# Performance work log

Measured on AMD Instinct MI355X. Metric: run time of the kernel, lower is better.

Reference implementation:

```python
import jax, jax.numpy as jnp
import numpy as np

N_NODES = 79
RAW_FEAT = 26
D_IN = RAW_FEAT + 6      # 32, in_channels after position concat
D_OUT = 2 * D_IN         # 64, out_channel_fac * in_channels
HIDDEN = 256
N_EDGES = 3000
BATCH = 256
POS_IDX = [120,124,128,132,136,140,144,148,152,237,241,245,249,253,257,261,265,269,354,358,362,366,370,374,378,382,386,471,475,479,483,487,491,495,499,503,588,592,596,600,604,608,612,616,620,705,709,713,717,721,725,729,733,737,822,826,830,834,838,842,846,850,854,48,53,60,67,73,157,352,388,583,586,817,901,906,913,920,926]


def _positions():
    width, height = 39, 25
    p = np.asarray(POS_IDX)
    xn = (p % width) / (width - 1)
    yn = (p // width) / (height - 1)
    feats = np.stack([xn, yn,
                      (np.sin(xn * 2 * np.pi) + 1) / 2,
                      (np.cos(xn * 2 * np.pi) + 1) / 2,
                      (np.sin(yn * 2 * np.pi) + 1) / 2,
                      (np.cos(yn * 2 * np.pi) + 1) / 2], axis=-1)
    return jnp.asarray(feats, jnp.float32)


def setup_inputs() -> dict:
    key = jax.random.key(0)
    ks = jax.random.split(key, 20)
    s = 0.05
    inp = {
        "state": jax.random.normal(ks[0], (BATCH, N_NODES, RAW_FEAT), jnp.float32),
        "pos_feat": _positions(),
        "edge_weights": jax.random.uniform(ks[1], (N_EDGES, 1), jnp.float32),
        # TransformerConv params (heads=1, edge_dim=1): torch Linear weights [out,in]
        "Wq": jax.random.normal(ks[2], (D_OUT, D_IN)) * s, "bq": jnp.zeros((D_OUT,)),
        "Wk": jax.random.normal(ks[3], (D_OUT, D_IN)) * s, "bk": jnp.zeros((D_OUT,)),
        "Wv": jax.random.normal(ks[4], (D_OUT, D_IN)) * s, "bv": jnp.zeros((D_OUT,)),
        "We": jax.random.normal(ks[5], (D_OUT, 1)) * s,            # lin_edge, bias=False
        "Wskip": jax.random.normal(ks[6], (D_OUT, D_IN)) * s, "bskip": jnp.zeros((D_OUT,)),
        # MLP head
        "W1": jax.random.normal(ks[7], (HIDDEN, D_IN + D_OUT + 1)) * s, "b1": jnp.zeros((HIDDEN,)),
        "g1": jnp.ones((HIDDEN,)), "beta1": jnp.zeros((HIDDEN,)),
        "W2": jax.random.normal(ks[8], (HIDDEN, HIDDEN)) * s, "b2": jnp.zeros((HIDDEN,)),
        "g2": jnp.ones((HIDDEN,)), "beta2": jnp.zeros((HIDDEN,)),
        "W3": jax.random.normal(ks[9], (1, HIDDEN)) * s, "b3": jnp.zeros((1,)),
        "edge_index": jax.random.randint(ks[10], (2, N_EDGES), 0, N_NODES, jnp.int32),
    }
    return inp


def _layernorm(x, g, b):
    m = x.mean(-1, keepdims=True)
    v = ((x - m) ** 2).mean(-1, keepdims=True)
    return (x - m) / jnp.sqrt(v + 1e-5) * g + b


def reference(state, pos_feat, edge_weights, Wq, bq, Wk, bk, Wv, bv, We, Wskip, bskip,
              W1, b1, g1, beta1, W2, b2, g2, beta2, W3, b3, edge_index):
    B = state.shape[0]
    # concat normalized positional features (shared across batch)
    x = jnp.concatenate([state, jnp.broadcast_to(pos_feat, (B, N_NODES, 6))], -1)  # [B,N,D_IN]
    src, dst = edge_index[0], edge_index[1]
    e = edge_weights @ We.T  # [E, D_OUT] edge embedding, shared across batch
    scale = 1.0 / jnp.sqrt(jnp.float32(D_OUT))

    def conv_one(xg):  # TransformerConv, heads=1, concat, root_weight
        q = xg @ Wq.T + bq
        k = xg @ Wk.T + bk
        v = xg @ Wv.T + bv
        ke = k[src] + e                      # [E, D_OUT]
        ve = v[src] + e
        alpha = (q[dst] * ke).sum(-1) * scale  # [E]
        amax = jax.ops.segment_max(alpha, dst, num_segments=N_NODES)
        amax = jnp.where(jnp.isfinite(amax), amax, 0.0)
        ex = jnp.exp(alpha - amax[dst])
        den = jax.ops.segment_sum(ex, dst, num_segments=N_NODES)
        w = ex / (den[dst] + 1e-16)
        agg = jax.ops.segment_sum(ve * w[:, None], dst, num_segments=N_NODES)
        return agg + xg @ Wskip.T + bskip

    out1 = jax.nn.relu(jax.vmap(conv_one)(x))  # [B,N,D_OUT]
    total_agents = x[..., 1].sum(-1)[:, None, None]  # [B,1,1]
    h = jnp.concatenate([out1, jnp.broadcast_to(total_agents, (B, N_NODES, 1)), x], -1)
    h = jax.nn.leaky_relu(_layernorm(h @ W1.T + b1, g1, beta1))
    h = jax.nn.leaky_relu(_layernorm(h @ W2.T + b2, g2, beta2))
    conc = jax.nn.softplus(h @ W3.T + b3).squeeze(-1)  # [B,N]
    action = conc / (conc.sum(-1, keepdims=True) + 1e-20)  # deterministic path
    return action
```

## Files before the change

### kernel.cpp

```cpp
#include <hip/hip_runtime.h>
#include <hip/hip_bf16.h>

#define N_NODES 79
#define RAW_FEAT 26
#define D_IN 32
#define D_OUT 64
#define HIDDEN 256
#define N_EDGES 3000
#define BATCH 256
#define M_ROWS (BATCH * N_NODES)
#define K1PAD 112

__global__ __launch_bounds__(256) void k_prep(
    const float* __restrict__ W1, const float* __restrict__ W2,
    const int* __restrict__ ei, const float* __restrict__ ew,
    const float* __restrict__ Wq, const float* __restrict__ Wk,
    const float* __restrict__ Wv, const float* __restrict__ Wsk,
    const float* __restrict__ bq, const float* __restrict__ bk,
    const float* __restrict__ bv, const float* __restrict__ bsk,
    float* __restrict__ W1t, float* __restrict__ W2t,
    float* __restrict__ Wall_t, float* __restrict__ ball,
    int* __restrict__ rp, int* __restrict__ csr_src,
    int* __restrict__ csr_dst, float* __restrict__ csr_ew)
{
    __shared__ float tile[64][65];
    __shared__ int cnt[N_NODES];
    __shared__ int base[N_NODES + 1];
    const int tid = threadIdx.x, bid = blockIdx.x;

    if (bid < 24) {
        const float* in; float* out; int C, Kpad, kb, rb;
        if (bid < 8) { in = W1; out = W1t; C = 97; Kpad = K1PAD;
                       kb = (bid & 1) * 64; rb = (bid >> 1) * 64; }
        else         { int b = bid - 8; in = W2; out = W2t; C = 256; Kpad = 256;
                       kb = (b & 3) * 64; rb = (b >> 2) * 64; }
        for (int i = tid; i < 4096; i += 256) {
            int rr = i >> 6, kk = i & 63;
            int r = rb + rr, k = kb + kk;
            tile[rr][kk] = (k < C) ? in[r * C + k] : 0.f;
        }
        __syncthreads();
        for (int i = tid; i < 4096; i += 256) {
            int kk = i >> 6, rr = i & 63;
            int k = kb + kk, r = rb + rr;
            if (k < Kpad) out[(size_t)k * HIDDEN + r] = tile[rr][kk];
        }
        return;
    }

    if (bid == 25) {
        for (int t = tid; t < 32 * 256; t += 256) {
            int k = t >> 8, j = t & 255;
            float v;
            if (j < 64)       v = Wq [j * 32 + k];
            else if (j < 128) v = Wk [(j - 64) * 32 + k];
            else if (j < 192) v = Wv [(j - 128) * 32 + k];
            else              v = Wsk[(j - 192) * 32 + k];
            Wall_t[t] = v;
        }
        if (tid < 64) {
            ball[tid]       = bq[tid];
            ball[64 + tid]  = bk[tid];
            ball[128 + tid] = bv[tid];
            ball[192 + tid] = bsk[tid];
        }
        return;
    }

    if (tid < N_NODES) cnt[tid] = 0;
    __syncthreads();
    for (int e = tid; e < N_EDGES; e += 256) atomicAdd(&cnt[ei[N_EDGES + e]], 1);
    __syncthreads();
    if (tid == 0) {
        int run = 0;
        for (int n = 0; n < N_NODES; ++n) { base[n] = run; run += cnt[n]; }
        base[N_NODES] = run;
    }
    __syncthreads();
    if (tid < N_NODES + 1) rp[tid] = base[tid];
    if (tid < N_NODES) cnt[tid] = base[tid];
    __syncthreads();
    for (int e = tid; e < N_EDGES; e += 256) {
        int d = ei[N_EDGES + e];
        int p = atomicAdd(&cnt[d], 1);
        csr_src[p] = ei[e];
        csr_dst[p] = d;
        csr_ew[p]  = ew[e];
    }
}

#define DOT4(S, Aa, Bb) S += Aa.x * Bb.x + Aa.y * Bb.y + Aa.z * Bb.z + Aa.w * Bb.w;

__global__ __launch_bounds__(512) void k1_conv(
    const float* __restrict__ state, const float* __restrict__ pos,
    const float* __restrict__ Wall_t, const float* __restrict__ ball,
    const int* __restrict__ rp_g, const int* __restrict__ csrc_g,
    const int* __restrict__ cdst_g, const float* __restrict__ cew_g,
    const float* __restrict__ We,
    float* __restrict__ out1_ws, float* __restrict__ ta_ws)
{
    __shared__ __align__(16) float qs [80 * 68];
    __shared__ __align__(16) float kss[80 * 68];
    __shared__ __align__(16) float vss[80 * 68];
    __shared__ __align__(16) float o1s[N_NODES * 68];
    __shared__ __align__(16) char uni[43904];
    __shared__ __align__(16) float ewc[N_EDGES];
    __shared__ unsigned short srcs[N_EDGES], dsts[N_EDGES];
    __shared__ __align__(16) float eW[64];
    __shared__ int   rp_s[80];
    __shared__ float qWe[80], csum_s[80];
    __shared__ float red80[80];

    float* xs     = (float*)uni;
    float* Wall_s = (float*)(uni + 10112);
    float* ball_s = (float*)(uni + 42880);
    float* SA     = (float*)uni;
    float* alpha  = (float*)(uni + 25600);

    const int b = blockIdx.x, tid = threadIdx.x;

    for (int t = tid; t < N_NODES * 32; t += 512) {
        int n = t >> 5, c = t & 31;
        xs[t] = (c < RAW_FEAT) ? state[(b * N_NODES + n) * RAW_FEAT + c]
                               : pos[n * 6 + (c - RAW_FEAT)];
    }
    {
        const float4* Wg4 = (const float4*)Wall_t;
        float4* Ws4w = (float4*)Wall_s;
        for (int t = tid; t < 2048; t += 512) Ws4w[t] = Wg4[t];
    }
    if (tid < 256) ball_s[tid] = ball[tid];
    for (int t = tid; t < N_EDGES; t += 512) {
        srcs[t] = (unsigned short)csrc_g[t];
        dsts[t] = (unsigned short)cdst_g[t];
        ewc[t]  = cew_g[t];
    }
    if (tid < 64) eW[tid] = We[tid];
    if (tid < 80) rp_s[tid] = rp_g[tid];
    if (tid < 79) red80[tid] = state[(b * N_NODES + tid) * RAW_FEAT + 1];
    if (tid == 79) red80[79] = 0.f;
    for (int t = tid; t < 68; t += 512) {
        qs[79 * 68 + t] = 0.f; kss[79 * 68 + t] = 0.f; vss[79 * 68 + t] = 0.f;
    }
    __syncthreads();

    {
        const float4* xs4 = (const float4*)xs;
        const float4* W4  = (const float4*)Wall_s;
        const float4* b4  = (const float4*)ball_s;
        for (int t = tid; t < N_NODES * 64; t += 512) {
            int n = t >> 6, c4 = t & 63;
            float4 acc = b4[c4];
            #pragma unroll
            for (int k4 = 0; k4 < 8; ++k4) {
                float4 xv = xs4[n * 8 + k4];
                float4 w0 = W4[(k4 * 4 + 0) * 64 + c4];
                float4 w1 = W4[(k4 * 4 + 1) * 64 + c4];
                float4 w2 = W4[(k4 * 4 + 2) * 64 + c4];
                float4 w3 = W4[(k4 * 4 + 3) * 64 + c4];
                acc.x += xv.x * w0.x + xv.y * w1.x + xv.z * w2.x + xv.w * w3.x;
                acc.y += xv.x * w0.y + xv.y * w1.y + xv.z * w2.y + xv.w * w3.y;
                acc.z += xv.x * w0.z + xv.y * w1.z + xv.z * w2.z + xv.w * w3.z;
                acc.w += xv.x * w0.w + xv.y * w1.w + xv.z * w2.w + xv.w * w3.w;
            }
            if (c4 < 16)      ((float4*)qs )[n * 17 + c4]        = acc;
            else if (c4 < 32) ((float4*)kss)[n * 17 + (c4 - 16)] = acc;
            else if (c4 < 48) ((float4*)vss)[n * 17 + (c4 - 32)] = acc;
            else              ((float4*)o1s)[n * 17 + (c4 - 48)] = acc;
        }
    }
    __syncthreads();

    for (int off = 64; off >= 1; off >>= 1) {
        if (tid < off && tid + off < 80) red80[tid] += red80[tid + off];
        __syncthreads();
    }
    if (tid == 0) ta_ws[b] = red80[0];
    if (tid < N_NODES) {
        const float4* q4 = (const float4*)(qs + tid * 68);
        const float4* e4 = (const float4*)eW;
        float s = 0.f;
        #pragma unroll
        for (int i = 0; i < 16; ++i) {
            float4 a = q4[i], e = e4[i];
            DOT4(s, a, e)
        }
        qWe[tid] = s;
    }
    __syncthreads();

    {
        const int rg = tid >> 5, cgp = tid & 31;
        const int r0 = rg * 5;
        int c0 = cgp * 3; if (c0 > 76) c0 = 76;
        float s00 = 0, s01 = 0, s02 = 0;
        float s10 = 0, s11 = 0, s12 = 0;
        float s20 = 0, s21 = 0, s22 = 0;
        float s30 = 0, s31 = 0, s32 = 0;
        float s40 = 0, s41 = 0, s42 = 0;
        const float4* q4p = (const float4*)qs;
        const float4* k4p = (const float4*)kss;
        for (int k4 = 0; k4 < 16; ++k4) {
            float4 q0 = q4p[(r0 + 0) * 17 + k4];
            float4 q1 = q4p[(r0 + 1) * 17 + k4];
            float4 q2 = q4p[(r0 + 2) * 17 + k4];
            float4 q3 = q4p[(r0 + 3) * 17 + k4];
            float4 q4v = q4p[(r0 + 4) * 17 + k4];
            float4 c0v = k4p[(c0 + 0) * 17 + k4];
            float4 c1v = k4p[(c0 + 1) * 17 + k4];
            float4 c2v = k4p[(c0 + 2) * 17 + k4];
            DOT4(s00, q0, c0v)  DOT4(s01, q0, c1v)  DOT4(s02, q0, c2v)
            DOT4(s10, q1, c0v)  DOT4(s11, q1, c1v)  DOT4(s12, q1, c2v)
            DOT4(s20, q2, c0v)  DOT4(s21, q2, c1v)  DOT4(s22, q2, c2v)
            DOT4(s30, q3, c0v)  DOT4(s31, q3, c1v)  DOT4(s32, q3, c2v)
            DOT4(s40, q4v, c0v) DOT4(s41, q4v, c1v) DOT4(s42, q4v, c2v)
        }
        SA[(r0 + 0) * 80 + c0 + 0] = s00; SA[(r0 + 0) * 80 + c0 + 1] = s01; SA[(r0 + 0) * 80 + c0 + 2] = s02;
        SA[(r0 + 1) * 80 + c0 + 0] = s10; SA[(r0 + 1) * 80 + c0 + 1] = s11; SA[(r0 + 1) * 80 + c0 + 2] = s12;
        SA[(r0 + 2) * 80 + c0 + 0] = s20; SA[(r0 + 2) * 80 + c0 + 1] = s21; SA[(r0 + 2) * 80 + c0 + 2] = s22;
        SA[(r0 + 3) * 80 + c0 + 0] = s30; SA[(r0 + 3) * 80 + c0 + 1] = s31; SA[(r0 + 3) * 80 + c0 + 2] = s32;
        SA[(r0 + 4) * 80 + c0 + 0] = s40; SA[(r0 + 4) * 80 + c0 + 1] = s41; SA[(r0 + 4) * 80 + c0 + 2] = s42;
    }
    __syncthreads();

    for (int t = tid; t < N_EDGES; t += 512) {
        int s = srcs[t], d = dsts[t];
        alpha[t] = 0.125f * (SA[d * 80 + s] + ewc[t] * qWe[d]);
    }
    __syncthreads();

    for (int t = tid; t < 6400; t += 512) SA[t] = 0.f;
    __syncthreads();

    if (tid < N_NODES) {
        int e0 = rp_s[tid], e1 = rp_s[tid + 1];
        float m = -1e30f;
        for (int e = e0; e < e1; ++e) m = fmaxf(m, alpha[e]);
        float s = 0.f, cs = 0.f;
        for (int e = e0; e < e1; ++e) {
            float ex = expf(alpha[e] - m);
            alpha[e] = ex;
            s += ex; cs += ex * ewc[e];
        }
        float rden = 1.f / (s + 1e-16f);
        csum_s[tid] = cs * rden;
        float* Ar = SA + tid * 80;
        for (int e = e0; e < e1; ++e) Ar[srcs[e]] += alpha[e] * rden;
    }
    __syncthreads();

    {
        const int rowg = tid >> 4, colg = tid & 15;
        int n0 = rowg * 3; if (n0 > 76) n0 = 76;
        float4 g0 = {0.f, 0.f, 0.f, 0.f};
        float4 g1 = {0.f, 0.f, 0.f, 0.f};
        float4 g2 = {0.f, 0.f, 0.f, 0.f};
        const float4* A4  = (const float4*)SA;
        const float4* v4p = (const float4*)vss;

#define AGGSTEP(COMP, SS) { \
        float4 vv = v4p[(s4 * 4 + SS) * 17 + colg]; \
        g0.x += a0.COMP * vv.x; g0.y += a0.COMP * vv.y; g0.z += a0.COMP * vv.z; g0.w += a0.COMP * vv.w; \
        g1.x += a1.COMP * vv.x; g1.y += a1.COMP * vv.y; g1.z += a1.COMP * vv.z; g1.w += a1.COMP * vv.w; \
        g2.x += a2.COMP * vv.x; g2.y += a2.COMP * vv.y; g2.z += a2.COMP * vv.z; g2.w += a2.COMP * vv.w; }

        for (int s4 = 0; s4 < 20; ++s4) {
            float4 a0 = A4[(n0 + 0) * 20 + s4];
            float4 a1 = A4[(n0 + 1) * 20 + s4];
            float4 a2 = A4[(n0 + 2) * 20 + s4];
            AGGSTEP(x, 0)
            AGGSTEP(y, 1)
            AGGSTEP(z, 2)
            AGGSTEP(w, 3)
        }
#undef AGGSTEP

        const float4* o4 = (const float4*)o1s;
        const float4* e4 = (const float4*)eW;
        float4 ev = e4[colg];

#define AGGOUT(GI, I) { int n = n0 + I; if (n < N_NODES) { \
        float4 sk = o4[n * 17 + colg]; float cs = csum_s[n]; float4 r; \
        r.x = fmaxf(sk.x + GI.x + cs * ev.x, 0.f); \
        r.y = fmaxf(sk.y + GI.y + cs * ev.y, 0.f); \
        r.z = fmaxf(sk.z + GI.z + cs * ev.z, 0.f); \
        r.w = fmaxf(sk.w + GI.w + cs * ev.w, 0.f); \
        ((float4*)out1_ws)[((size_t)b * N_NODES + n) * 16 + colg] = r; } }

        AGGOUT(g0, 0)
        AGGOUT(g1, 1)
        AGGOUT(g2, 2)
#undef AGGOUT
    }
}

__global__ __launch_bounds__(256) void k23_mlp(
    const float* __restrict__ state, const float* __restrict__ pos,
    const float* __restrict__ out1_ws, const float* __restrict__ ta_ws,
    const float* __restrict__ W1t, const float* __restrict__ b1,
    const float* __restrict__ g1, const float* __restrict__ be1,
    const float* __restrict__ W2t, const float* __restrict__ b2,
    const float* __restrict__ g2, const float* __restrict__ be2,
    const float* __restrict__ W3, const float* __restrict__ b3,
    float* __restrict__ conc_ws)
{
    __shared__ __align__(16) float A12[32 * 256];
    __shared__ __align__(16) float Ws[16 * 256];

    const int tid = threadIdx.x;
    const int cg = tid & 31;
    const int rg = tid >> 5;
    const int m0 = blockIdx.x * 32;

    const float4* W1t4 = (const float4*)W1t;
    const float4* W2t4 = (const float4*)W2t;
    const float4* A12_4 = (const float4*)A12;
    float4* Ws4w = (float4*)Ws;
    const float4* Ws4 = (const float4*)Ws;

    for (int t = tid; t < 32 * K1PAD; t += 256) {
        int r = t / K1PAD, k = t - r * K1PAD;
        int m = m0 + r;
        float v = 0.f;
        if (k < 64)       v = out1_ws[m * 64 + k];
        else if (k == 64) v = ta_ws[m / N_NODES];
        else if (k < 91)  v = state[m * RAW_FEAT + (k - 65)];
        else if (k < 97)  { int n = m - (m / N_NODES) * N_NODES;
                            v = pos[n * 6 + (k - 91)]; }
        A12[t] = v;
    }
    float4 pre0 = W1t4[tid];
    float4 pre1 = W1t4[tid + 256];
    float4 pre2 = W1t4[tid + 512];
    float4 pre3 = W1t4[tid + 768];
    __syncthreads();

    float4 accL0 = {0,0,0,0}, accL1 = {0,0,0,0}, accL2 = {0,0,0,0}, accL3 = {0,0,0,0};
    float4 accH0 = {0,0,0,0}, accH1 = {0,0,0,0}, accH2 = {0,0,0,0}, accH3 = {0,0,0,0};

#define KSTEP(COMP, KS) { \
    float4 wL = Ws4[(kq * 4 + KS) * 64 + cg]; \
    float4 wH = Ws4[(kq * 4 + KS) * 64 + 32 + cg]; \
    accL0.x += a0.COMP * wL.x; accL0.y += a0.COMP * wL.y; accL0.z += a0.COMP * wL.z; accL0.w += a0.COMP * wL.w; \
    accL1.x += a1.COMP * wL.x; accL1.y += a1.COMP * wL.y; accL1.z += a1.COMP * wL.z; accL1.w += a1.COMP * wL.w; \
    accL2.x += a2.COMP * wL.x; accL2.y += a2.COMP * wL.y; accL2.z += a2.COMP * wL.z; accL2.w += a2.COMP * wL.w; \
    accL3.x += a3.COMP * wL.x; accL3.y += a3.COMP * wL.y; accL3.z += a3.COMP * wL.z; accL3.w += a3.COMP * wL.w; \
    accH0.x += a0.COMP * wH.x; accH0.y += a0.COMP * wH.y; accH0.z += a0.COMP * wH.z; accH0.w += a0.COMP * wH.w; \
    accH1.x += a1.COMP * wH.x; accH1.y += a1.COMP * wH.y; accH1.z += a1.COMP * wH.z; accH1.w += a1.COMP * wH.w; \
    accH2.x += a2.COMP * wH.x; accH2.y += a2.COMP * wH.y; accH2.z += a2.COMP * wH.z; accH2.w += a2.COMP * wH.w; \
    accH3.x += a3.COMP * wH.x; accH3.y += a3.COMP * wH.y; accH3.z += a3.COMP * wH.z; accH3.w += a3.COMP * wH.w; }

    for (int ch = 0; ch < 7; ++ch) {
        Ws4w[tid] = pre0; Ws4w[tid + 256] = pre1;
        Ws4w[tid + 512] = pre2; Ws4w[tid + 768] = pre3;
        __syncthreads();
        if (ch < 6) {
            pre0 = W1t4[(ch + 1) * 1024 + tid];
            pre1 = W1t4[(ch + 1) * 1024 + tid + 256];
            pre2 = W1t4[(ch + 1) * 1024 + tid + 512];
            pre3 = W1t4[(ch + 1) * 1024 + tid + 768];
        } else {
            pre0 = W2t4[tid];
            pre1 = W2t4[tid + 256];
            pre2 = W2t4[tid + 512];
            pre3 = W2t4[tid + 768];
        }
        #pragma unroll
        for (int kq = 0; kq < 4; ++kq) {
            float4 a0 = A12_4[(rg * 4 + 0) * 28 + ch * 4 + kq];
            float4 a1 = A12_4[(rg * 4 + 1) * 28 + ch * 4 + kq];
            float4 a2 = A12_4[(rg * 4 + 2) * 28 + ch * 4 + kq];
            float4 a3 = A12_4[(rg * 4 + 3) * 28 + ch * 4 + kq];
            KSTEP(x, 0)
            KSTEP(y, 1)
            KSTEP(z, 2)
            KSTEP(w, 3)
        }
        __syncthreads();
    }

    {
        float4 bL = ((const float4*)b1)[cg],  bH = ((const float4*)b1)[32 + cg];
        float4 gL = ((const float4*)g1)[cg],  gH = ((const float4*)g1)[32 + cg];
        float4 eL = ((const float4*)be1)[cg], eH = ((const float4*)be1)[32 + cg];

#define LN1_ROW(AL, AH, RR) { \
        float v0 = AL.x + bL.x, v1 = AL.y + bL.y, v2 = AL.z + bL.z, v3 = AL.w + bL.w; \
        float v4 = AH.x + bH.x, v5 = AH.y + bH.y, v6 = AH.z + bH.z, v7 = AH.w + bH.w; \
        float sm = v0 + v1 + v2 + v3 + v4 + v5 + v6 + v7; \
        float sq = v0*v0 + v1*v1 + v2*v2 + v3*v3 + v4*v4 + v5*v5 + v6*v6 + v7*v7; \
        for (int off = 16; off >= 1; off >>= 1) { sm += __shfl_xor(sm, off, 64); sq += __shfl_xor(sq, off, 64); } \
        float mu = sm * (1.f / 256.f), rstd = rsqrtf(sq * (1.f / 256.f) - mu * mu + 1e-5f); \
        float4 yL, yH; \
        yL.x = (v0 - mu) * rstd * gL.x + eL.x; yL.y = (v1 - mu) * rstd * gL.y + eL.y; \
        yL.z = (v2 - mu) * rstd * gL.z + eL.z; yL.w = (v3 - mu) * rstd * gL.w + eL.w; \
        yH.x = (v4 - mu) * rstd * gH.x + eH.x; yH.y = (v5 - mu) * rstd * gH.y + eH.y; \
        yH.z = (v6 - mu) * rstd * gH.z + eH.z; yH.w = (v7 - mu) * rstd * gH.w + eH.w; \
        yL.x = yL.x > 0.f ? yL.x : 0.01f * yL.x; yL.y = yL.y > 0.f ? yL.y : 0.01f * yL.y; \
        yL.z = yL.z > 0.f ? yL.z : 0.01f * yL.z; yL.w = yL.w > 0.f ? yL.w : 0.01f * yL.w; \
        yH.x = yH.x > 0.f ? yH.x : 0.01f * yH.x; yH.y = yH.y > 0.f ? yH.y : 0.01f * yH.y; \
        yH.z = yH.z > 0.f ? yH.z : 0.01f * yH.z; yH.w = yH.w > 0.f ? yH.w : 0.01f * yH.w; \
        ((float4*)A12)[(rg * 4 + RR) * 64 + cg] = yL; \
        ((float4*)A12)[(rg * 4 + RR) * 64 + 32 + cg] = yH; }

        LN1_ROW(accL0, accH0, 0)
        LN1_ROW(accL1, accH1, 1)
        LN1_ROW(accL2, accH2, 2)
        LN1_ROW(accL3, accH3, 3)
#undef LN1_ROW
        accL0 = {0,0,0,0}; accL1 = {0,0,0,0}; accL2 = {0,0,0,0}; accL3 = {0,0,0,0};
        accH0 = {0,0,0,0}; accH1 = {0,0,0,0}; accH2 = {0,0,0,0}; accH3 = {0,0,0,0};
    }

    for (int ch = 0; ch < 16; ++ch) {
        Ws4w[tid] = pre0; Ws4w[tid + 256] = pre1;
        Ws4w[tid + 512] = pre2; Ws4w[tid + 768] = pre3;
        __syncthreads();
        if (ch < 15) {
            pre0 = W2t4[(ch + 1) * 1024 + tid];
            pre1 = W2t4[(ch + 1) * 1024 + tid + 256];
            pre2 = W2t4[(ch + 1) * 1024 + tid + 512];
            pre3 = W2t4[(ch + 1) * 1024 + tid + 768];
        }
        #pragma unroll
        for (int kq = 0; kq < 4; ++kq) {
            float4 a0 = A12_4[(rg * 4 + 0) * 64 + ch * 4 + kq];
            float4 a1 = A12_4[(rg * 4 + 1) * 64 + ch * 4 + kq];
            float4 a2 = A12_4[(rg * 4 + 2) * 64 + ch * 4 + kq];
            float4 a3 = A12_4[(rg * 4 + 3) * 64 + ch * 4 + kq];
            KSTEP(x, 0)
            KSTEP(y, 1)
            KSTEP(z, 2)
            KSTEP(w, 3)
        }
        __syncthreads();
    }
#undef KSTEP

    {
        float4 bL = ((const float4*)b2)[cg],  bH = ((const float4*)b2)[32 + cg];
        float4 gL = ((const float4*)g2)[cg],  gH = ((const float4*)g2)[32 + cg];
        float4 eL = ((const float4*)be2)[cg], eH = ((const float4*)be2)[32 + cg];
        float4 wL3 = ((const float4*)W3)[cg], wH3 = ((const float4*)W3)[32 + cg];
        float bb3 = b3[0];

#define LN2_ROW(AL, AH, RR) { \
        float v0 = AL.x + bL.x, v1 = AL.y + bL.y, v2 = AL.z + bL.z, v3 = AL.w + bL.w; \
        float v4 = AH.x + bH.x, v5 = AH.y + bH.y, v6 = AH.z + bH.z, v7 = AH.w + bH.w; \
        float sm = v0 + v1 + v2 + v3 + v4 + v5 + v6 + v7; \
        float sq = v0*v0 + v1*v1 + v2*v2 + v3*v3 + v4*v4 + v5*v5 + v6*v6 + v7*v7; \
        for (int off = 16; off >= 1; off >>= 1) { sm += __shfl_xor(sm, off, 64); sq += __shfl_xor(sq, off, 64); } \
        float mu = sm * (1.f / 256.f), rstd = rsqrtf(sq * (1.f / 256.f) - mu * mu + 1e-5f); \
        float z0 = (v0 - mu) * rstd * gL.x + eL.x, z1 = (v1 - mu) * rstd * gL.y + eL.y; \
        float z2 = (v2 - mu) * rstd * gL.z + eL.z, z3 = (v3 - mu) * rstd * gL.w + eL.w; \
        float z4 = (v4 - mu) * rstd * gH.x + eH.x, z5 = (v5 - mu) * rstd * gH.y + eH.y; \
        float z6 = (v6 - mu) * rstd * gH.z + eH.z, z7 = (v7 - mu) * rstd * gH.w + eH.w; \
        z0 = z0 > 0.f ? z0 : 0.01f * z0; z1 = z1 > 0.f ? z1 : 0.01f * z1; \
        z2 = z2 > 0.f ? z2 : 0.01f * z2; z3 = z3 > 0.f ? z3 : 0.01f * z3; \
        z4 = z4 > 0.f ? z4 : 0.01f * z4; z5 = z5 > 0.f ? z5 : 0.01f * z5; \
        z6 = z6 > 0.f ? z6 : 0.01f * z6; z7 = z7 > 0.f ? z7 : 0.01f * z7; \
        float part = z0 * wL3.x + z1 * wL3.y + z2 * wL3.z + z3 * wL3.w \
                   + z4 * wH3.x + z5 * wH3.y + z6 * wH3.z + z7 * wH3.w; \
        for (int off = 16; off >= 1; off >>= 1) part += __shfl_xor(part, off, 64); \
        if (cg == 0) { float x = part + bb3; \
            conc_ws[m0 + rg * 4 + RR] = fmaxf(x, 0.f) + log1pf(expf(-fabsf(x))); } }

        LN2_ROW(accL0, accH0, 0)
        LN2_ROW(accL1, accH1, 1)
        LN2_ROW(accL2, accH2, 2)
        LN2_ROW(accL3, accH3, 3)
#undef LN2_ROW
    }
}

__global__ __launch_bounds__(128) void k4_norm(
    const float* __restrict__ conc_ws, float* __restrict__ out)
{
    __shared__ float red[128];
    const int b = blockIdx.x, tid = threadIdx.x;
    float v = 0.f;
    if (tid < N_NODES) v = conc_ws[b * N_NODES + tid];
    red[tid] = v;
    __syncthreads();
    for (int off = 64; off >= 1; off >>= 1) {
        if (tid < off) red[tid] += red[tid + off];
        __syncthreads();
    }
    float s = red[0];
    if (tid < N_NODES) out[b * N_NODES + tid] = v / (s + 1e-20f);
}

extern "C" void kernel_launch(void* const* d_in, const int* in_sizes, int n_in,
                              void* d_out, int out_size, void* d_ws, size_t ws_size,
                              hipStream_t stream) {
    const float* state = (const float*)d_in[0];
    const float* pos   = (const float*)d_in[1];
    const float* ew    = (const float*)d_in[2];
    const float* Wq  = (const float*)d_in[3];  const float* bq  = (const float*)d_in[4];
    const float* Wk  = (const float*)d_in[5];  const float* bk  = (const float*)d_in[6];
    const float* Wv  = (const float*)d_in[7];  const float* bv  = (const float*)d_in[8];
    const float* We  = (const float*)d_in[9];
    const float* Wsk = (const float*)d_in[10]; const float* bsk = (const float*)d_in[11];
    const float* W1  = (const float*)d_in[12]; const float* b1  = (const float*)d_in[13];
    const float* g1  = (const float*)d_in[14]; const float* be1 = (const float*)d_in[15];
    const float* W2  = (const float*)d_in[16]; const float* b2  = (const float*)d_in[17];
    const float* g2  = (const float*)d_in[18]; const float* be2 = (const float*)d_in[19];
    const float* W3  = (const float*)d_in[20]; const float* b3  = (const float*)d_in[21];
    const int*   ei  = (const int*)d_in[22];

    float* ws    = (float*)d_ws;
    float* ta    = ws;
    float* out1  = ws + 256;
    float* conc  = out1 + (size_t)M_ROWS * 64;
    float* W1t   = conc + M_ROWS;
    float* W2t   = W1t + K1PAD * HIDDEN;
    float* Wall  = W2t + HIDDEN * HIDDEN;
    float* ball  = Wall + 32 * 256;
    int*   rp    = (int*)(ball + 256);
    int*   csrc  = rp + 80;
    int*   cdst  = csrc + N_EDGES;
    float* cew   = (float*)(cdst + N_EDGES);
    float* out   = (float*)d_out;

    k_prep<<<dim3(26), dim3(256), 0, stream>>>(
        W1, W2, ei, ew, Wq, Wk, Wv, Wsk, bq, bk, bv, bsk,
        W1t, W2t, Wall, ball, rp, csrc, cdst, cew);
    k1_conv<<<dim3(BATCH), dim3(512), 0, stream>>>(
        state, pos, Wall, ball, rp, csrc, cdst, cew, We, out1, ta);
    k23_mlp<<<dim3(M_ROWS / 32), dim3(256), 0, stream>>>(
        state, pos, out1, ta, W1t, b1, g1, be1,
        W2t, b2, g2, be2, W3, b3, conc);
    k4_norm<<<dim3(BATCH), dim3(128), 0, stream>>>(conc, out);
}
```

Measured before the change: 220.4 us.

## Read MLP weights directly from global memory and halve rows per block

The MLP kernel no longer stages W1/W2 chunks through shared memory with register prefetch and per-chunk barriers. Each thread now reads weight float4s straight from global memory (L2/L1 cached), and each block handles 16 rows instead of 32, doubling the grid and cutting LDS use. This removes most __syncthreads and the shared-memory staging, and raises occupancy. In exchange, weight reuse per fetch drops by half and every weight access goes through the cache hierarchy, which could make the kernel bound on global/L2 bandwidth.

```diff
diff --git a/kernel.cpp b/kernel.cpp
--- a/kernel.cpp
+++ b/kernel.cpp
@@ -304,21 +304,18 @@
     const float* __restrict__ W3, const float* __restrict__ b3,
     float* __restrict__ conc_ws)
 {
-    __shared__ __align__(16) float A12[32 * 256];
-    __shared__ __align__(16) float Ws[16 * 256];
+    __shared__ __align__(16) float A12[16 * 256];
 
     const int tid = threadIdx.x;
     const int cg = tid & 31;
     const int rg = tid >> 5;
-    const int m0 = blockIdx.x * 32;
+    const int m0 = blockIdx.x * 16;
 
     const float4* W1t4 = (const float4*)W1t;
     const float4* W2t4 = (const float4*)W2t;
     const float4* A12_4 = (const float4*)A12;
-    float4* Ws4w = (float4*)Ws;
-    const float4* Ws4 = (const float4*)Ws;
-
-    for (int t = tid; t < 32 * K1PAD; t += 256) {
+
+    for (int t = tid; t < 16 * K1PAD; t += 256) {
         int r = t / K1PAD, k = t - r * K1PAD;
         int m = m0 + r;
         float v = 0.f;
@@ -329,55 +326,29 @@
                             v = pos[n * 6 + (k - 91)]; }
         A12[t] = v;
     }
-    float4 pre0 = W1t4[tid];
-    float4 pre1 = W1t4[tid + 256];
-    float4 pre2 = W1t4[tid + 512];
-    float4 pre3 = W1t4[tid + 768];
-    __syncthreads();
-
-    float4 accL0 = {0,0,0,0}, accL1 = {0,0,0,0}, accL2 = {0,0,0,0}, accL3 = {0,0,0,0};
-    float4 accH0 = {0,0,0,0}, accH1 = {0,0,0,0}, accH2 = {0,0,0,0}, accH3 = {0,0,0,0};
-
-#define KSTEP(COMP, KS) { \
-    float4 wL = Ws4[(kq * 4 + KS) * 64 + cg]; \
-    float4 wH = Ws4[(kq * 4 + KS) * 64 + 32 + cg]; \
+    __syncthreads();
+
+    float4 accL0 = {0,0,0,0}, accL1 = {0,0,0,0};
+    float4 accH0 = {0,0,0,0}, accH1 = {0,0,0,0};
+
+#define KSTEP(WMAT, COMP, KIDX) { \
+    float4 wL = WMAT[(KIDX) * 64 + cg]; \
+    float4 wH = WMAT[(KIDX) * 64 + 32 + cg]; \
     accL0.x += a0.COMP * wL.x; accL0.y += a0.COMP * wL.y; accL0.z += a0.COMP * wL.z; accL0.w += a0.COMP * wL.w; \
     accL1.x += a1.COMP * wL.x; accL1.y += a1.COMP * wL.y; accL1.z += a1.COMP * wL.z; accL1.w += a1.COMP * wL.w; \
-    accL2.x += a2.COMP * wL.x; accL2.y += a2.COMP * wL.y; accL2.z += a2.COMP * wL.z; accL2.w += a2.COMP * wL.w; \
-    accL3.x += a3.COMP * wL.x; accL3.y += a3.COMP * wL.y; accL3.z += a3.COMP * wL.z; accL3.w += a3.COMP * wL.w; \
     accH0.x += a0.COMP * wH.x; accH0.y += a0.COMP * wH.y; accH0.z += a0.COMP * wH.z; accH0.w += a0.COMP * wH.w; \
-    accH1.x += a1.COMP * wH.x; accH1.y += a1.COMP * wH.y; accH1.z += a1.COMP * wH.z; accH1.w += a1.COMP * wH.w; \
-    accH2.x += a2.COMP * wH.x; accH2.y += a2.COMP * wH.y; accH2.z += a2.COMP * wH.z; accH2.w += a2.COMP * wH.w; \
-    accH3.x += a3.COMP * wH.x; accH3.y += a3.COMP * wH.y; accH3.z += a3.COMP * wH.z; accH3.w += a3.COMP * wH.w; }
-
-    for (int ch = 0; ch < 7; ++ch) {
-        Ws4w[tid] = pre0; Ws4w[tid + 256] = pre1;
-        Ws4w[tid + 512] = pre2; Ws4w[tid + 768] = pre3;
-        __syncthreads();
-        if (ch < 6) {
-            pre0 = W1t4[(ch + 1) * 1024 + tid];
-            pre1 = W1t4[(ch + 1) * 1024 + tid + 256];
-            pre2 = W1t4[(ch + 1) * 1024 + tid + 512];
-            pre3 = W1t4[(ch + 1) * 1024 + tid + 768];
-        } else {
-            pre0 = W2t4[tid];
-            pre1 = W2t4[tid + 256];
-            pre2 = W2t4[tid + 512];
-            pre3 = W2t4[tid + 768];
-        }
-        #pragma unroll
-        for (int kq = 0; kq < 4; ++kq) {
-            float4 a0 = A12_4[(rg * 4 + 0) * 28 + ch * 4 + kq];
-            float4 a1 = A12_4[(rg * 4 + 1) * 28 + ch * 4 + kq];
-            float4 a2 = A12_4[(rg * 4 + 2) * 28 + ch * 4 + kq];
-            float4 a3 = A12_4[(rg * 4 + 3) * 28 + ch * 4 + kq];
-            KSTEP(x, 0)
-            KSTEP(y, 1)
-            KSTEP(z, 2)
-            KSTEP(w, 3)
-        }
-        __syncthreads();
-    }
+    accH1.x += a1.COMP * wH.x; accH1.y += a1.COMP * wH.y; accH1.z += a1.COMP * wH.z; accH1.w += a1.COMP * wH.w; }
+
+    #pragma unroll 4
+    for (int k4 = 0; k4 < 28; ++k4) {
+        float4 a0 = A12_4[(rg * 2 + 0) * 28 + k4];
+        float4 a1 = A12_4[(rg * 2 + 1) * 28 + k4];
+        KSTEP(W1t4, x, k4 * 4 + 0)
+        KSTEP(W1t4, y, k4 * 4 + 1)
+        KSTEP(W1t4, z, k4 * 4 + 2)
+        KSTEP(W1t4, w, k4 * 4 + 3)
+    }
+    __syncthreads();
 
     {
         float4 bL = ((const float4*)b1)[cg],  bH = ((const float4*)b1)[32 + cg];
@@ -400,40 +371,25 @@
         yL.z = yL.z > 0.f ? yL.z : 0.01f * yL.z; yL.w = yL.w > 0.f ? yL.w : 0.01f * yL.w; \
         yH.x = yH.x > 0.f ? yH.x : 0.01f * yH.x; yH.y = yH.y > 0.f ? yH.y : 0.01f * yH.y; \
         yH.z = yH.z > 0.f ? yH.z : 0.01f * yH.z; yH.w = yH.w > 0.f ? yH.w : 0.01f * yH.w; \
-        ((float4*)A12)[(rg * 4 + RR) * 64 + cg] = yL; \
-        ((float4*)A12)[(rg * 4 + RR) * 64 + 32 + cg] = yH; }
+        ((float4*)A12)[(rg * 2 + RR) * 64 + cg] = yL; \
+        ((float4*)A12)[(rg * 2 + RR) * 64 + 32 + cg] = yH; }
 
         LN1_ROW(accL0, accH0, 0)
         LN1_ROW(accL1, accH1, 1)
-        LN1_ROW(accL2, accH2, 2)
-        LN1_ROW(accL3, accH3, 3)
 #undef LN1_ROW
-        accL0 = {0,0,0,0}; accL1 = {0,0,0,0}; accL2 = {0,0,0,0}; accL3 = {0,0,0,0};
-        accH0 = {0,0,0,0}; accH1 = {0,0,0,0}; accH2 = {0,0,0,0}; accH3 = {0,0,0,0};
-    }
-
-    for (int ch = 0; ch < 16; ++ch) {
-        Ws4w[tid] = pre0; Ws4w[tid + 256] = pre1;
-        Ws4w[tid + 512] = pre2; Ws4w[tid + 768] = pre3;
-        __syncthreads();
-        if (ch < 15) {
-            pre0 = W2t4[(ch + 1) * 1024 + tid];
-            pre1 = W2t4[(ch + 1) * 1024 + tid + 256];
-            pre2 = W2t4[(ch + 1) * 1024 + tid + 512];
-            pre3 = W2t4[(ch + 1) * 1024 + tid + 768];
-        }
-        #pragma unroll
-        for (int kq = 0; kq < 4; ++kq) {
-            float4 a0 = A12_4[(rg * 4 + 0) * 64 + ch * 4 + kq];
-            float4 a1 = A12_4[(rg * 4 + 1) * 64 + ch * 4 + kq];
-            float4 a2 = A12_4[(rg * 4 + 2) * 64 + ch * 4 + kq];
-            float4 a3 = A12_4[(rg * 4 + 3) * 64 + ch * 4 + kq];
-            KSTEP(x, 0)
-            KSTEP(y, 1)
-            KSTEP(z, 2)
-            KSTEP(w, 3)
-        }
-        __syncthreads();
+        accL0 = {0,0,0,0}; accL1 = {0,0,0,0};
+        accH0 = {0,0,0,0}; accH1 = {0,0,0,0};
+    }
+    __syncthreads();
+
+    #pragma unroll 4
+    for (int k4 = 0; k4 < 64; ++k4) {
+        float4 a0 = A12_4[(rg * 2 + 0) * 64 + k4];
+        float4 a1 = A12_4[(rg * 2 + 1) * 64 + k4];
+        KSTEP(W2t4, x, k4 * 4 + 0)
+        KSTEP(W2t4, y, k4 * 4 + 1)
+        KSTEP(W2t4, z, k4 * 4 + 2)
+        KSTEP(W2t4, w, k4 * 4 + 3)
     }
 #undef KSTEP
 
@@ -463,12 +419,10 @@
                    + z4 * wH3.x + z5 * wH3.y + z6 * wH3.z + z7 * wH3.w; \
         for (int off = 16; off >= 1; off >>= 1) part += __shfl_xor(part, off, 64); \
         if (cg == 0) { float x = part + bb3; \
-            conc_ws[m0 + rg * 4 + RR] = fmaxf(x, 0.f) + log1pf(expf(-fabsf(x))); } }
+            conc_ws[m0 + rg * 2 + RR] = fmaxf(x, 0.f) + log1pf(expf(-fabsf(x))); } }
 
         LN2_ROW(accL0, accH0, 0)
         LN2_ROW(accL1, accH1, 1)
-        LN2_ROW(accL2, accH2, 2)
-        LN2_ROW(accL3, accH3, 3)
 #undef LN2_ROW
     }
 }
@@ -527,7 +481,7 @@
         W1t, W2t, Wall, ball, rp, csrc, cdst, cew);
     k1_conv<<<dim3(BATCH), dim3(512), 0, stream>>>(
         state, pos, Wall, ball, rp, csrc, cdst, cew, We, out1, ta);
-    k23_mlp<<<dim3(M_ROWS / 32), dim3(256), 0, stream>>>(
+    k23_mlp<<<dim3(M_ROWS / 16), dim3(256), 0, stream>>>(
         state, pos, out1, ta, W1t, b1, g1, be1,
         W2t, b2, g2, be2, W3, b3, conc);
     k4_norm<<<dim3(BATCH), dim3(128), 0, stream>>>(conc, out);
```

New measurement: 253.4 us. 1.15x slower.

## Double-buffer MLP weight tiles and widen conv kernel to 1024 threads

Applied to the files above, without the earlier changes.

The MLP kernel now keeps two shared-memory weight buffers. The next chunk is written into the idle buffer after the current chunk's compute, which removes one barrier per chunk. Separately, the graph-conv kernel moves from 512 to 1024 threads per block, with each thread doing smaller pieces of the attention-score and aggregation work (3x3 and 2-row tiles). The 1024-thread blocks may lower register budgets and occupancy, and the doubled weight buffer uses more LDS per MLP block.

```diff
diff --git a/kernel.cpp b/kernel.cpp
--- a/kernel.cpp
+++ b/kernel.cpp
@@ -91,7 +91,7 @@
 
 #define DOT4(S, Aa, Bb) S += Aa.x * Bb.x + Aa.y * Bb.y + Aa.z * Bb.z + Aa.w * Bb.w;
 
-__global__ __launch_bounds__(512) void k1_conv(
+__global__ __launch_bounds__(1024) void k1_conv(
     const float* __restrict__ state, const float* __restrict__ pos,
     const float* __restrict__ Wall_t, const float* __restrict__ ball,
     const int* __restrict__ rp_g, const int* __restrict__ csrc_g,
@@ -119,7 +119,7 @@
 
     const int b = blockIdx.x, tid = threadIdx.x;
 
-    for (int t = tid; t < N_NODES * 32; t += 512) {
+    for (int t = tid; t < N_NODES * 32; t += 1024) {
         int n = t >> 5, c = t & 31;
         xs[t] = (c < RAW_FEAT) ? state[(b * N_NODES + n) * RAW_FEAT + c]
                                : pos[n * 6 + (c - RAW_FEAT)];
@@ -127,10 +127,10 @@
     {
         const float4* Wg4 = (const float4*)Wall_t;
         float4* Ws4w = (float4*)Wall_s;
-        for (int t = tid; t < 2048; t += 512) Ws4w[t] = Wg4[t];
+        for (int t = tid; t < 2048; t += 1024) Ws4w[t] = Wg4[t];
     }
     if (tid < 256) ball_s[tid] = ball[tid];
-    for (int t = tid; t < N_EDGES; t += 512) {
+    for (int t = tid; t < N_EDGES; t += 1024) {
         srcs[t] = (unsigned short)csrc_g[t];
         dsts[t] = (unsigned short)cdst_g[t];
         ewc[t]  = cew_g[t];
@@ -139,7 +139,7 @@
     if (tid < 80) rp_s[tid] = rp_g[tid];
     if (tid < 79) red80[tid] = state[(b * N_NODES + tid) * RAW_FEAT + 1];
     if (tid == 79) red80[79] = 0.f;
-    for (int t = tid; t < 68; t += 512) {
+    for (int t = tid; t < 68; t += 1024) {
         qs[79 * 68 + t] = 0.f; kss[79 * 68 + t] = 0.f; vss[79 * 68 + t] = 0.f;
     }
     __syncthreads();
@@ -148,7 +148,7 @@
         const float4* xs4 = (const float4*)xs;
         const float4* W4  = (const float4*)Wall_s;
         const float4* b4  = (const float4*)ball_s;
-        for (int t = tid; t < N_NODES * 64; t += 512) {
+        for (int t = tid; t < N_NODES * 64; t += 1024) {
             int n = t >> 6, c4 = t & 63;
             float4 acc = b4[c4];
             #pragma unroll
@@ -190,46 +190,38 @@
     __syncthreads();
 
     {
-        const int rg = tid >> 5, cgp = tid & 31;
-        const int r0 = rg * 5;
-        int c0 = cgp * 3; if (c0 > 76) c0 = 76;
+        const int rowg = tid >> 5, cgp = tid & 31;
+        int r0 = rowg * 3; if (r0 > 77) r0 = 77;
+        int c0 = cgp * 3;  if (c0 > 76) c0 = 76;
         float s00 = 0, s01 = 0, s02 = 0;
         float s10 = 0, s11 = 0, s12 = 0;
         float s20 = 0, s21 = 0, s22 = 0;
-        float s30 = 0, s31 = 0, s32 = 0;
-        float s40 = 0, s41 = 0, s42 = 0;
         const float4* q4p = (const float4*)qs;
         const float4* k4p = (const float4*)kss;
         for (int k4 = 0; k4 < 16; ++k4) {
             float4 q0 = q4p[(r0 + 0) * 17 + k4];
             float4 q1 = q4p[(r0 + 1) * 17 + k4];
             float4 q2 = q4p[(r0 + 2) * 17 + k4];
-            float4 q3 = q4p[(r0 + 3) * 17 + k4];
-            float4 q4v = q4p[(r0 + 4) * 17 + k4];
             float4 c0v = k4p[(c0 + 0) * 17 + k4];
             float4 c1v = k4p[(c0 + 1) * 17 + k4];
             float4 c2v = k4p[(c0 + 2) * 17 + k4];
             DOT4(s00, q0, c0v)  DOT4(s01, q0, c1v)  DOT4(s02, q0, c2v)
             DOT4(s10, q1, c0v)  DOT4(s11, q1, c1v)  DOT4(s12, q1, c2v)
             DOT4(s20, q2, c0v)  DOT4(s21, q2, c1v)  DOT4(s22, q2, c2v)
-            DOT4(s30, q3, c0v)  DOT4(s31, q3, c1v)  DOT4(s32, q3, c2v)
-            DOT4(s40, q4v, c0v) DOT4(s41, q4v, c1v) DOT4(s42, q4v, c2v)
         }
         SA[(r0 + 0) * 80 + c0 + 0] = s00; SA[(r0 + 0) * 80 + c0 + 1] = s01; SA[(r0 + 0) * 80 + c0 + 2] = s02;
         SA[(r0 + 1) * 80 + c0 + 0] = s10; SA[(r0 + 1) * 80 + c0 + 1] = s11; SA[(r0 + 1) * 80 + c0 + 2] = s12;
         SA[(r0 + 2) * 80 + c0 + 0] = s20; SA[(r0 + 2) * 80 + c0 + 1] = s21; SA[(r0 + 2) * 80 + c0 + 2] = s22;
-        SA[(r0 + 3) * 80 + c0 + 0] = s30; SA[(r0 + 3) * 80 + c0 + 1] = s31; SA[(r0 + 3) * 80 + c0 + 2] = s32;
-        SA[(r0 + 4) * 80 + c0 + 0] = s40; SA[(r0 + 4) * 80 + c0 + 1] = s41; SA[(r0 + 4) * 80 + c0 + 2] = s42;
-    }
-    __syncthreads();
-
-    for (int t = tid; t < N_EDGES; t += 512) {
+    }
+    __syncthreads();
+
+    for (int t = tid; t < N_EDGES; t += 1024) {
         int s = srcs[t], d = dsts[t];
         alpha[t] = 0.125f * (SA[d * 80 + s] + ewc[t] * qWe[d]);
     }
     __syncthreads();
 
-    for (int t = tid; t < 6400; t += 512) SA[t] = 0.f;
+    for (int t = tid; t < 6400; t += 1024) SA[t] = 0.f;
     __syncthreads();
 
     if (tid < N_NODES) {
@@ -251,46 +243,44 @@
 
     {
         const int rowg = tid >> 4, colg = tid & 15;
-        int n0 = rowg * 3; if (n0 > 76) n0 = 76;
-        float4 g0 = {0.f, 0.f, 0.f, 0.f};
-        float4 g1 = {0.f, 0.f, 0.f, 0.f};
-        float4 g2 = {0.f, 0.f, 0.f, 0.f};
-        const float4* A4  = (const float4*)SA;
-        const float4* v4p = (const float4*)vss;
+        if (rowg < 40) {
+            const int n0 = rowg * 2;
+            float4 g0 = {0.f, 0.f, 0.f, 0.f};
+            float4 g1 = {0.f, 0.f, 0.f, 0.f};
+            const float4* A4  = (const float4*)SA;
+            const float4* v4p = (const float4*)vss;
 
 #define AGGSTEP(COMP, SS) { \
-        float4 vv = v4p[(s4 * 4 + SS) * 17 + colg]; \
-        g0.x += a0.COMP * vv.x; g0.y += a0.COMP * vv.y; g0.z += a0.COMP * vv.z; g0.w += a0.COMP * vv.w; \
-        g1.x += a1.COMP * vv.x; g1.y += a1.COMP * vv.y; g1.z += a1.COMP * vv.z; g1.w += a1.COMP * vv.w; \
-        g2.x += a2.COMP * vv.x; g2.y += a2.COMP * vv.y; g2.z += a2.COMP * vv.z; g2.w += a2.COMP * vv.w; }
-
-        for (int s4 = 0; s4 < 20; ++s4) {
-            float4 a0 = A4[(n0 + 0) * 20 + s4];
-            float4 a1 = A4[(n0 + 1) * 20 + s4];
-            float4 a2 = A4[(n0 + 2) * 20 + s4];
-            AGGSTEP(x, 0)
-            AGGSTEP(y, 1)
-            AGGSTEP(z, 2)
-            AGGSTEP(w, 3)
-        }
+            float4 vv = v4p[(s4 * 4 + SS) * 17 + colg]; \
+            g0.x += a0.COMP * vv.x; g0.y += a0.COMP * vv.y; g0.z += a0.COMP * vv.z; g0.w += a0.COMP * vv.w; \
+            g1.x += a1.COMP * vv.x; g1.y += a1.COMP * vv.y; g1.z += a1.COMP * vv.z; g1.w += a1.COMP * vv.w; }
+
+            for (int s4 = 0; s4 < 20; ++s4) {
+                float4 a0 = A4[(n0 + 0) * 20 + s4];
+                float4 a1 = A4[(n0 + 1) * 20 + s4];
+                AGGSTEP(x, 0)
+                AGGSTEP(y, 1)
+                AGGSTEP(z, 2)
+                AGGSTEP(w, 3)
+            }
 #undef AGGSTEP
 
-        const float4* o4 = (const float4*)o1s;
-        const float4* e4 = (const float4*)eW;
-        float4 ev = e4[colg];
+            const float4* o4 = (const float4*)o1s;
+            const float4* e4 = (const float4*)eW;
+            float4 ev = e4[colg];
 
 #define AGGOUT(GI, I) { int n = n0 + I; if (n < N_NODES) { \
-        float4 sk = o4[n * 17 + colg]; float cs = csum_s[n]; float4 r; \
-        r.x = fmaxf(sk.x + GI.x + cs * ev.x, 0.f); \
-        r.y = fmaxf(sk.y + GI.y + cs * ev.y, 0.f); \
-        r.z = fmaxf(sk.z + GI.z + cs * ev.z, 0.f); \
-        r.w = fmaxf(sk.w + GI.w + cs * ev.w, 0.f); \
-        ((float4*)out1_ws)[((size_t)b * N_NODES + n) * 16 + colg] = r; } }
-
-        AGGOUT(g0, 0)
-        AGGOUT(g1, 1)
-        AGGOUT(g2, 2)
+            float4 sk = o4[n * 17 + colg]; float cs = csum_s[n]; float4 r; \
+            r.x = fmaxf(sk.x + GI.x + cs * ev.x, 0.f); \
+            r.y = fmaxf(sk.y + GI.y + cs * ev.y, 0.f); \
+            r.z = fmaxf(sk.z + GI.z + cs * ev.z, 0.f); \
+            r.w = fmaxf(sk.w + GI.w + cs * ev.w, 0.f); \
+            ((float4*)out1_ws)[((size_t)b * N_NODES + n) * 16 + colg] = r; } }
+
+            AGGOUT(g0, 0)
+            AGGOUT(g1, 1)
 #undef AGGOUT
+        }
     }
 }
 
@@ -305,7 +295,7 @@
     float* __restrict__ conc_ws)
 {
     __shared__ __align__(16) float A12[32 * 256];
-    __shared__ __align__(16) float Ws[16 * 256];
+    __shared__ __align__(16) float Ws[2][16 * 256];
 
     const int tid = threadIdx.x;
     const int cg = tid & 31;
@@ -315,8 +305,6 @@
     const float4* W1t4 = (const float4*)W1t;
     const float4* W2t4 = (const float4*)W2t;
     const float4* A12_4 = (const float4*)A12;
-    float4* Ws4w = (float4*)Ws;
-    const float4* Ws4 = (const float4*)Ws;
 
     for (int t = tid; t < 32 * K1PAD; t += 256) {
         int r = t / K1PAD, k = t - r * K1PAD;
@@ -329,18 +317,25 @@
                             v = pos[n * 6 + (k - 91)]; }
         A12[t] = v;
     }
-    float4 pre0 = W1t4[tid];
-    float4 pre1 = W1t4[tid + 256];
-    float4 pre2 = W1t4[tid + 512];
-    float4 pre3 = W1t4[tid + 768];
+
+    float4 p0, p1, p2, p3;
+#define LOADJ(J) { const float4* _s = ((J) < 7) ? (W1t4 + (J) * 1024) \
+                                                : (W2t4 + ((J) - 7) * 1024); \
+    p0 = _s[tid]; p1 = _s[tid + 256]; p2 = _s[tid + 512]; p3 = _s[tid + 768]; }
+#define WRITEWS(B) { float4* _d = (float4*)Ws[(B)]; \
+    _d[tid] = p0; _d[tid + 256] = p1; _d[tid + 512] = p2; _d[tid + 768] = p3; }
+
+    LOADJ(0)
+    WRITEWS(0)
+    LOADJ(1)
     __syncthreads();
 
     float4 accL0 = {0,0,0,0}, accL1 = {0,0,0,0}, accL2 = {0,0,0,0}, accL3 = {0,0,0,0};
     float4 accH0 = {0,0,0,0}, accH1 = {0,0,0,0}, accH2 = {0,0,0,0}, accH3 = {0,0,0,0};
 
 #define KSTEP(COMP, KS) { \
-    float4 wL = Ws4[(kq * 4 + KS) * 64 + cg]; \
-    float4 wH = Ws4[(kq * 4 + KS) * 64 + 32 + cg]; \
+    float4 wL = Wc[(kq * 4 + KS) * 64 + cg]; \
+    float4 wH = Wc[(kq * 4 + KS) * 64 + 32 + cg]; \
     accL0.x += a0.COMP * wL.x; accL0.y += a0.COMP * wL.y; accL0.z += a0.COMP * wL.z; accL0.w += a0.COMP * wL.w; \
     accL1.x += a1.COMP * wL.x; accL1.y += a1.COMP * wL.y; accL1.z += a1.COMP * wL.z; accL1.w += a1.COMP * wL.w; \
     accL2.x += a2.COMP * wL.x; accL2.y += a2.COMP * wL.y; accL2.z += a2.COMP * wL.z; accL2.w += a2.COMP * wL.w; \
@@ -350,32 +345,21 @@
     accH2.x += a2.COMP * wH.x; accH2.y += a2.COMP * wH.y; accH2.z += a2.COMP * wH.z; accH2.w += a2.COMP * wH.w; \
     accH3.x += a3.COMP * wH.x; accH3.y += a3.COMP * wH.y; accH3.z += a3.COMP * wH.z; accH3.w += a3.COMP * wH.w; }
 
-    for (int ch = 0; ch < 7; ++ch) {
-        Ws4w[tid] = pre0; Ws4w[tid + 256] = pre1;
-        Ws4w[tid + 512] = pre2; Ws4w[tid + 768] = pre3;
-        __syncthreads();
-        if (ch < 6) {
-            pre0 = W1t4[(ch + 1) * 1024 + tid];
-            pre1 = W1t4[(ch + 1) * 1024 + tid + 256];
-            pre2 = W1t4[(ch + 1) * 1024 + tid + 512];
-            pre3 = W1t4[(ch + 1) * 1024 + tid + 768];
-        } else {
-            pre0 = W2t4[tid];
-            pre1 = W2t4[tid + 256];
-            pre2 = W2t4[tid + 512];
-            pre3 = W2t4[tid + 768];
-        }
+    for (int j = 0; j < 7; ++j) {
+        const float4* Wc = (const float4*)Ws[j & 1];
         #pragma unroll
         for (int kq = 0; kq < 4; ++kq) {
-            float4 a0 = A12_4[(rg * 4 + 0) * 28 + ch * 4 + kq];
-            float4 a1 = A12_4[(rg * 4 + 1) * 28 + ch * 4 + kq];
-            float4 a2 = A12_4[(rg * 4 + 2) * 28 + ch * 4 + kq];
-            float4 a3 = A12_4[(rg * 4 + 3) * 28 + ch * 4 + kq];
+            float4 a0 = A12_4[(rg * 4 + 0) * 28 + j * 4 + kq];
+            float4 a1 = A12_4[(rg * 4 + 1) * 28 + j * 4 + kq];
+            float4 a2 = A12_4[(rg * 4 + 2) * 28 + j * 4 + kq];
+            float4 a3 = A12_4[(rg * 4 + 3) * 28 + j * 4 + kq];
             KSTEP(x, 0)
             KSTEP(y, 1)
             KSTEP(z, 2)
             KSTEP(w, 3)
         }
+        WRITEWS((j + 1) & 1)
+        LOADJ(j + 2)
         __syncthreads();
     }
 
@@ -411,31 +395,30 @@
         accL0 = {0,0,0,0}; accL1 = {0,0,0,0}; accL2 = {0,0,0,0}; accL3 = {0,0,0,0};
         accH0 = {0,0,0,0}; accH1 = {0,0,0,0}; accH2 = {0,0,0,0}; accH3 = {0,0,0,0};
     }
-
-    for (int ch = 0; ch < 16; ++ch) {
-        Ws4w[tid] = pre0; Ws4w[tid + 256] = pre1;
-        Ws4w[tid + 512] = pre2; Ws4w[tid + 768] = pre3;
-        __syncthreads();
-        if (ch < 15) {
-            pre0 = W2t4[(ch + 1) * 1024 + tid];
-            pre1 = W2t4[(ch + 1) * 1024 + tid + 256];
-            pre2 = W2t4[(ch + 1) * 1024 + tid + 512];
-            pre3 = W2t4[(ch + 1) * 1024 + tid + 768];
-        }
+    __syncthreads();
+
+    for (int jj = 0; jj < 16; ++jj) {
+        const float4* Wc = (const float4*)Ws[(jj + 1) & 1];
         #pragma unroll
         for (int kq = 0; kq < 4; ++kq) {
-            float4 a0 = A12_4[(rg * 4 + 0) * 64 + ch * 4 + kq];
-            float4 a1 = A12_4[(rg * 4 + 1) * 64 + ch * 4 + kq];
-            float4 a2 = A12_4[(rg * 4 + 2) * 64 + ch * 4 + kq];
-            float4 a3 = A12_4[(rg * 4 + 3) * 64 + ch * 4 + kq];
+            float4 a0 = A12_4[(rg * 4 + 0) * 64 + jj * 4 + kq];
+            float4 a1 = A12_4[(rg * 4 + 1) * 64 + jj * 4 + kq];
+            float4 a2 = A12_4[(rg * 4 + 2) * 64 + jj * 4 + kq];
+            float4 a3 = A12_4[(rg * 4 + 3) * 64 + jj * 4 + kq];
             KSTEP(x, 0)
             KSTEP(y, 1)
             KSTEP(z, 2)
             KSTEP(w, 3)
         }
-        __syncthreads();
+        if (jj < 15) {
+            WRITEWS(jj & 1)
+            if (jj < 14) LOADJ(jj + 9)
+            __syncthreads();
+        }
     }
 #undef KSTEP
+#undef LOADJ
+#undef WRITEWS
 
     {
         float4 bL = ((const float4*)b2)[cg],  bH = ((const float4*)b2)[32 + cg];
@@ -525,7 +508,7 @@
     k_prep<<<dim3(26), dim3(256), 0, stream>>>(
         W1, W2, ei, ew, Wq, Wk, Wv, Wsk, bq, bk, bv, bsk,
         W1t, W2t, Wall, ball, rp, csrc, cdst, cew);
-    k1_conv<<<dim3(BATCH), dim3(512), 0, stream>>>(
+    k1_conv<<<dim3(BATCH), dim3(1024), 0, stream>>>(
         state, pos, Wall, ball, rp, csrc, cdst, cew, We, out1, ta);
     k23_mlp<<<dim3(M_ROWS / 32), dim3(256), 0, stream>>>(
         state, pos, out1, ta, W1t, b1, g1, be1,
```

Result: slower. 341.9 us (+55.1%).
